# Optimization experiments

Hardware: AMD Instinct MI355X
Metric: run time of the kernel (lower is better)

Reference implementation:

```python
import jax, jax.numpy as jnp
import numpy as np
import math

DIM = 2048
N_HEADS = 16
HEAD_DIM = DIM // N_HEADS  # 128
SEQ = 2048
EPS = 1e-5
NEG = -1e9


def get_slopes(n):
    # n is a power of 2 here (16)
    start = 2.0 ** (-2.0 ** (-(math.log2(n) - 3)))
    return [start * start ** i for i in range(n)]


def setup_inputs() -> dict:
    key = jax.random.key(0)
    ks = jax.random.split(key, 6)
    x = jax.random.normal(ks[0], (1, SEQ, DIM), dtype=jnp.float32)
    # causal additive mask (large negative above diagonal)
    causal = jnp.tril(jnp.ones((SEQ, SEQ), dtype=bool))
    mask = jnp.where(causal, 0.0, NEG).astype(jnp.float32)[None, None]
    scale_w = 0.02
    wq = jax.random.normal(ks[1], (DIM, DIM), dtype=jnp.float32) * scale_w  # [in, out]
    wk = jax.random.normal(ks[2], (DIM, DIM), dtype=jnp.float32) * scale_w
    wv = jax.random.normal(ks[3], (DIM, DIM), dtype=jnp.float32) * scale_w
    wo = jax.random.normal(ks[4], (DIM, DIM), dtype=jnp.float32) * scale_w
    # AttentionPrior params: shape_init=1, scale_init='slope' (stored as log), loc_init=0
    shape = jnp.ones((1, N_HEADS, 1, 1), dtype=jnp.float32)
    scale = jnp.log(jnp.asarray(get_slopes(N_HEADS), dtype=jnp.float32)).reshape(1, N_HEADS, 1, 1)
    loc = jnp.zeros((1, N_HEADS, 1, 1), dtype=jnp.float32)
    return {"x": x, "mask": mask, "wq": wq, "wk": wk, "wv": wv, "wo": wo,
            "shape": shape, "scale": scale, "loc": loc, "start_pos": 0}


def _prior_bias(shape, scale, loc, seqlen, start_pos):
    q_pos = jnp.arange(seqlen, dtype=jnp.float32) + start_pos
    k_pos = jnp.arange(seqlen + start_pos, dtype=jnp.float32)
    dist = (k_pos[None, :] - q_pos[:, None])[None, None]  # [1,1,S,K]
    loc_t = jnp.exp(loc) - jnp.exp(-loc)
    z = (dist - loc_t) * jnp.exp(scale)  # [1,H,S,K]
    return -(jnp.abs(z) + EPS) ** shape


def reference(x, mask, wq, wk, wv, wo, shape, scale, loc, start_pos):
    bsz, seqlen, _ = x.shape
    q = (x @ wq).reshape(bsz, seqlen, N_HEADS, HEAD_DIM)
    k = (x @ wk).reshape(bsz, seqlen, N_HEADS, HEAD_DIM)
    v = (x @ wv).reshape(bsz, seqlen, N_HEADS, HEAD_DIM)
    # start_pos=0 prefill: cache slice == current keys/values
    scores = jnp.einsum('bqhd,bkhd->bhqk', q, k) / math.sqrt(HEAD_DIM)
    scores = scores + _prior_bias(shape, scale, loc, seqlen, start_pos)
    scores = scores + mask
    probs = jax.nn.softmax(scores.astype(jnp.float32), axis=-1).astype(q.dtype)
    out = jnp.einsum('bhqk,bkhd->bqhd', probs, v).reshape(bsz, seqlen, DIM)
    return out @ wo
```

## Files before the change

kernel.cpp:

```cpp
#include <hip/hip_runtime.h>
#include <hip/hip_bf16.h>
#include <stdint.h>


typedef unsigned short u16;
typedef unsigned int u32;

using bf16x8 = __attribute__((ext_vector_type(8))) __bf16;
using f32x4  = __attribute__((ext_vector_type(4))) float;

__device__ __forceinline__ u16 f2bf(float f) {
  union { float f; u32 u; } v; v.f = f;
  u32 r = (v.u + 0x7FFFu + ((v.u >> 16) & 1u)) >> 16;
  return (u16)r;
}

__device__ __forceinline__ float bf2f(u16 h) {
  union { u32 u; float f; } v; v.u = ((u32)h) << 16; return v.f;
}

__device__ __forceinline__ void gload16(const void* g, void* l) {
  __builtin_amdgcn_global_load_lds((const __attribute__((address_space(1))) void*)g,
                                   (__attribute__((address_space(3))) void*)l, 16, 0, 0);
}

__device__ __forceinline__ int cumchunks(int qt) {
  if (qt < 8)  return qt;
  if (qt < 16) return 8 + 2 * (qt - 8);
  if (qt < 24) return 24 + 3 * (qt - 16);
  return 48 + 4 * (qt - 24);
}

__global__ __launch_bounds__(256) void prep(const float* __restrict__ x, const float* __restrict__ wq,
                                            const float* __restrict__ wk, const float* __restrict__ wv,
                                            const float* __restrict__ wo,
                                            u16* __restrict__ xb, u16* __restrict__ wqkt,
                                            u16* __restrict__ wvt, u16* __restrict__ wot) {
  __shared__ float tile[32][33];
  const int z = blockIdx.z;
  const int t = threadIdx.x;
  if (z == 4) {
    int i = ((blockIdx.y * 64 + blockIdx.x) * 256 + t);
    float4 v = ((const float4*)x)[i];
    ushort4 o;
    o.x = f2bf(v.x); o.y = f2bf(v.y); o.z = f2bf(v.z); o.w = f2bf(v.w);
    ((ushort4*)xb)[i] = o;
    return;
  }
  const float* src = (z == 0) ? wq : (z == 1) ? wk : (z == 2) ? wv : wo;
  u16* dst = (z == 0) ? wqkt : (z == 1) ? (wqkt + 2048 * 2048) : (z == 2) ? wvt : wot;
  const int c0 = blockIdx.x * 32, r0 = blockIdx.y * 32;
  const int ci = t & 31, rj = t >> 5;
#pragma unroll
  for (int j = 0; j < 4; ++j)
    tile[rj + j * 8][ci] = src[(size_t)(r0 + rj + j * 8) * 2048 + c0 + ci];
  __syncthreads();
#pragma unroll
  for (int j = 0; j < 4; ++j) {
    int rr = rj + j * 8;
    dst[(size_t)(c0 + rr) * 2048 + r0 + ci] = f2bf(tile[ci][rr]);
  }
}

__global__ __launch_bounds__(256) void gemm_qkv(const u16* __restrict__ xb, const u16* __restrict__ wqkt,
                                                const u16* __restrict__ wvt,
                                                u16* __restrict__ qkc, u16* __restrict__ vtc) {
  __shared__ u16 lds[16384];
  int bid = blockIdx.x;
  const u16 *A, *Bt;
  u16* C;
  int N, bn, bm, scl_cols;
  if (bid < 512) { A = xb;  Bt = wqkt; C = qkc; N = 4096; bn = bid & 31; bm = bid >> 5; scl_cols = 2048; }
  else { bid -= 512; A = wvt; Bt = xb; C = vtc; N = 2048; bn = bid & 15; bm = bid >> 4; scl_cols = 0; }
  const int K = 2048;

  const int t = threadIdx.x;
  const int w = t >> 6, l = t & 63;
  const int wm = w >> 1, wn = w & 1;
  const int lrow = l & 15, lgrp = l >> 4;

  f32x4 acc[4][4] = {};

  for (int k0 = 0; k0 < K; k0 += 64) {
    if (k0) __syncthreads();
#pragma unroll
    for (int p = 0; p < 4; ++p) {
      int i = (p * 4 + w) * 64 + l;
      int r = i >> 3, u = i & 7;
      const u16* src = A + (size_t)(bm * 128 + r) * K + k0 + ((u ^ (r & 7)) << 3);
      gload16(src, (char*)lds + (p * 4 + w) * 1024);
    }
#pragma unroll
    for (int p = 0; p < 4; ++p) {
      int i = (p * 4 + w) * 64 + l;
      int r = i >> 3, u = i & 7;
      const u16* src = Bt + (size_t)(bn * 128 + r) * K + k0 + ((u ^ (r & 7)) << 3);
      gload16(src, (char*)lds + 16384 + (p * 4 + w) * 1024);
    }
    __syncthreads();

#pragma unroll
    for (int kc = 0; kc < 2; ++kc) {
      bf16x8 af[4], bfr[4];
#pragma unroll
      for (int mt = 0; mt < 4; ++mt) {
        int rho = wm * 64 + mt * 16 + lrow;
        int un = (kc * 4 + lgrp) ^ (rho & 7);
        af[mt] = *(const bf16x8*)((const char*)lds + rho * 128 + un * 16);
      }
#pragma unroll
      for (int nt = 0; nt < 4; ++nt) {
        int rho = wn * 64 + nt * 16 + lrow;
        int un = (kc * 4 + lgrp) ^ (rho & 7);
        bfr[nt] = *(const bf16x8*)((const char*)lds + 16384 + rho * 128 + un * 16);
      }
#pragma unroll
      for (int mt = 0; mt < 4; ++mt)
#pragma unroll
        for (int nt = 0; nt < 4; ++nt)
          acc[mt][nt] = __builtin_amdgcn_mfma_f32_16x16x32_bf16(af[mt], bfr[nt], acc[mt][nt], 0, 0, 0);
    }
  }

  const int row0 = bm * 128 + wm * 64;
  const int col0 = bn * 128 + wn * 64;
#pragma unroll
  for (int mt = 0; mt < 4; ++mt)
#pragma unroll
    for (int nt = 0; nt < 4; ++nt) {
      int col = col0 + nt * 16 + lrow;
      float s = (col < scl_cols) ? 0.08838834764831843f : 1.0f;
#pragma unroll
      for (int r = 0; r < 4; ++r) {
        int row = row0 + mt * 16 + lgrp * 4 + r;
        C[(size_t)row * N + col] = f2bf(acc[mt][nt][r] * s);
      }
    }
}

__global__ __launch_bounds__(256) void gemm_outk(const u16* __restrict__ A, const u16* __restrict__ Bt,
                                                 u16* __restrict__ P0, u16* __restrict__ P1) {
  __shared__ u16 lds[16384];
  const int b = blockIdx.x;
  const int z = b >> 8;
  const int bn = b & 15, bm = (b >> 4) & 15;
  u16* C = z ? P1 : P0;
  const int K = 2048;
  const int kbeg = z * 1024, kend = kbeg + 1024;

  const int t = threadIdx.x;
  const int w = t >> 6, l = t & 63;
  const int wm = w >> 1, wn = w & 1;
  const int lrow = l & 15, lgrp = l >> 4;

  f32x4 acc[4][4] = {};

  for (int k0 = kbeg; k0 < kend; k0 += 64) {
    if (k0 != kbeg) __syncthreads();
#pragma unroll
    for (int p = 0; p < 4; ++p) {
      int i = (p * 4 + w) * 64 + l;
      int r = i >> 3, u = i & 7;
      const u16* src = A + (size_t)(bm * 128 + r) * K + k0 + ((u ^ (r & 7)) << 3);
      gload16(src, (char*)lds + (p * 4 + w) * 1024);
    }
#pragma unroll
    for (int p = 0; p < 4; ++p) {
      int i = (p * 4 + w) * 64 + l;
      int r = i >> 3, u = i & 7;
      const u16* src = Bt + (size_t)(bn * 128 + r) * K + k0 + ((u ^ (r & 7)) << 3);
      gload16(src, (char*)lds + 16384 + (p * 4 + w) * 1024);
    }
    __syncthreads();

#pragma unroll
    for (int kc = 0; kc < 2; ++kc) {
      bf16x8 af[4], bfr[4];
#pragma unroll
      for (int mt = 0; mt < 4; ++mt) {
        int rho = wm * 64 + mt * 16 + lrow;
        int un = (kc * 4 + lgrp) ^ (rho & 7);
        af[mt] = *(const bf16x8*)((const char*)lds + rho * 128 + un * 16);
      }
#pragma unroll
      for (int nt = 0; nt < 4; ++nt) {
        int rho = wn * 64 + nt * 16 + lrow;
        int un = (kc * 4 + lgrp) ^ (rho & 7);
        bfr[nt] = *(const bf16x8*)((const char*)lds + 16384 + rho * 128 + un * 16);
      }
#pragma unroll
      for (int mt = 0; mt < 4; ++mt)
#pragma unroll
        for (int nt = 0; nt < 4; ++nt)
          acc[mt][nt] = __builtin_amdgcn_mfma_f32_16x16x32_bf16(af[mt], bfr[nt], acc[mt][nt], 0, 0, 0);
    }
  }

  const int row0 = bm * 128 + wm * 64;
  const int col0 = bn * 128 + wn * 64;
#pragma unroll
  for (int mt = 0; mt < 4; ++mt)
#pragma unroll
    for (int nt = 0; nt < 4; ++nt) {
      int col = col0 + nt * 16 + lrow;
#pragma unroll
      for (int r = 0; r < 4; ++r) {
        int row = row0 + mt * 16 + lgrp * 4 + r;
        C[(size_t)row * 2048 + col] = f2bf(acc[mt][nt][r]);
      }
    }
}

__global__ __launch_bounds__(256) void combine_out(const u16* __restrict__ P0, const u16* __restrict__ P1,
                                                   float* __restrict__ out) {
  const int i = blockIdx.x * 256 + threadIdx.x;
  uint4 a = ((const uint4*)P0)[i];
  uint4 b = ((const uint4*)P1)[i];
  float4 o0, o1;
  o0.x = bf2f(a.x & 0xFFFF) + bf2f(b.x & 0xFFFF); o0.y = bf2f(a.x >> 16) + bf2f(b.x >> 16);
  o0.z = bf2f(a.y & 0xFFFF) + bf2f(b.y & 0xFFFF); o0.w = bf2f(a.y >> 16) + bf2f(b.y >> 16);
  o1.x = bf2f(a.z & 0xFFFF) + bf2f(b.z & 0xFFFF); o1.y = bf2f(a.z >> 16) + bf2f(b.z >> 16);
  o1.z = bf2f(a.w & 0xFFFF) + bf2f(b.w & 0xFFFF); o1.w = bf2f(a.w >> 16) + bf2f(b.w >> 16);
  ((float4*)out)[i * 2]     = o0;
  ((float4*)out)[i * 2 + 1] = o1;
}

__global__ __launch_bounds__(256) void attn_part(const u16* __restrict__ QK, const u16* __restrict__ Vt,
                                                 u16* __restrict__ Opart, float* __restrict__ Lpart,
                                                 const float* __restrict__ g_shape,
                                                 const float* __restrict__ g_scale,
                                                 const float* __restrict__ g_loc,
                                                 const int* __restrict__ g_sp) {
  __shared__ u16 k_lds[2][4096];
  __shared__ u16 v_lds[2][4096];
  __shared__ u16 p_lds[4][640];

  const int raw = blockIdx.x;
  const int bid = (raw & 7) * 160 + (raw >> 3);
  const int h = bid / 80;
  const int rem = bid - h * 80;
  int qt, ch;
  if (rem < 8)       { qt = rem;                 ch = 0; }
  else if (rem < 24) { int r2 = rem - 8;  qt = 8  + (r2 >> 1); ch = r2 & 1; }
  else if (rem < 48) { int r3 = rem - 24; qt = 16 + r3 / 3;    ch = r3 - 3 * (r3 / 3); }
  else               { int r4 = rem - 48; qt = 24 + (r4 >> 2); ch = r4 & 3; }
  const int pid = bid;

  const int t = threadIdx.x, w = t >> 6, l = t & 63;
  const int lrow = l & 15, lgrp = l >> 4;

  const float sh = g_shape[h];
  const float es = __expf(g_scale[h]);
  const float lcv = g_loc[h];
  const float loc_t = __expf(lcv) - __expf(-lcv);
  const int sp = g_sp[0];
  const bool shape1 = (sh == 1.0f);

  const int qbase = qt * 64 + w * 16;

  bf16x8 qf[4];
  {
    const u16* qp = QK + (size_t)(qbase + lrow) * 4096 + h * 128 + lgrp * 8;
#pragma unroll
    for (int kc = 0; kc < 4; ++kc) qf[kc] = *(const bf16x8*)(qp + kc * 32);
  }

  f32x4 o[8] = {};
  float lr[4] = {0.0f, 0.0f, 0.0f, 0.0f};

  const int kstart = ch * 16;
  const int kend = min(kstart + 16, 2 * qt + 2);

#define STAGE_TILE(buf, kt_) do {                                                        \
    const int kv0s = (kt_) * 32;                                                         \
    _Pragma("unroll")                                                                    \
    for (int p = 0; p < 2; ++p) {                                                        \
      int i = p * 256 + t;                                                               \
      int r = i >> 4, u = i & 15;                                                        \
      const u16* src = QK + (size_t)(kv0s + r) * 4096 + 2048 + h * 128 + ((u ^ (r & 7)) << 3); \
      gload16(src, (char*)k_lds[buf] + (p * 256 + w * 64) * 16);                         \
    }                                                                                    \
    _Pragma("unroll")                                                                    \
    for (int p = 0; p < 2; ++p) {                                                        \
      int i = p * 256 + t;                                                               \
      int r = i >> 2, u = i & 3;                                                         \
      const u16* src = Vt + (size_t)(h * 128 + r) * 2048 + kv0s + ((u ^ ((r >> 2) & 3)) << 3); \
      gload16(src, (char*)v_lds[buf] + (p * 256 + w * 64) * 16);                         \
    }                                                                                    \
  } while (0)

  STAGE_TILE(0, kstart);
  __syncthreads();

  for (int kt = kstart; kt < kend; ++kt) {
    const int cur = (kt - kstart) & 1;
    if (kt + 1 < kend) STAGE_TILE(cur ^ 1, kt + 1);
    const int kv0 = kt * 32;

    f32x4 s4[2];
#pragma unroll
    for (int nc = 0; nc < 2; ++nc) s4[nc] = f32x4{-11.0f, -11.0f, -11.0f, -11.0f};
#pragma unroll
    for (int kc = 0; kc < 4; ++kc) {
#pragma unroll
      for (int nc = 0; nc < 2; ++nc) {
        int rho = nc * 16 + lrow;
        int un = (kc * 4 + lgrp) ^ (rho & 7);
        bf16x8 bk = *(const bf16x8*)((const char*)k_lds[cur] + rho * 256 + un * 16);
        s4[nc] = __builtin_amdgcn_mfma_f32_16x16x32_bf16(qf[kc], bk, s4[nc], 0, 0, 0);
      }
    }

    f32x4 p4[2];
    const bool need_mask = (kv0 + 31 > qbase + sp);
    if (shape1 && !need_mask) {
#pragma unroll
      for (int r = 0; r < 4; ++r) {
        const float fb = (float)(kv0 + lrow - (qbase + lgrp * 4 + r) - sp) - loc_t;
#pragma unroll
        for (int nc = 0; nc < 2; ++nc) {
          float u = fb + (float)(nc * 16);
          float p = __expf(fmaf(-es, fabsf(u), s4[nc][r]));
          p4[nc][r] = p;
          lr[r] += p;
        }
      }
    } else if (shape1) {
#pragma unroll
      for (int r = 0; r < 4; ++r) {
        const float fb = (float)(kv0 + lrow - (qbase + lgrp * 4 + r) - sp) - loc_t;
#pragma unroll
        for (int nc = 0; nc < 2; ++nc) {
          float u = fb + (float)(nc * 16);
          float p = __expf(fmaf(-es, fabsf(u), s4[nc][r]));
          p = (u + loc_t > 0.0f) ? 0.0f : p;
          p4[nc][r] = p;
          lr[r] += p;
        }
      }
    } else {
#pragma unroll
      for (int r = 0; r < 4; ++r) {
        const float fb = (float)(kv0 + lrow - (qbase + lgrp * 4 + r) - sp) - loc_t;
#pragma unroll
        for (int nc = 0; nc < 2; ++nc) {
          float u = fb + (float)(nc * 16);
          float az = fmaf(es, fabsf(u), 1e-5f);
          float p = __expf(s4[nc][r] - __powf(az, sh));
          p = (u + loc_t > 0.0f) ? 0.0f : p;
          p4[nc][r] = p;
          lr[r] += p;
        }
      }
    }

#pragma unroll
    for (int r = 0; r < 4; ++r)
#pragma unroll
      for (int nc = 0; nc < 2; ++nc)
        p_lds[w][(lgrp * 4 + r) * 40 + nc * 16 + lrow] = f2bf(p4[nc][r]);

    {
      bf16x8 pa = *(const bf16x8*)((const char*)p_lds[w] + lrow * 80 + lgrp * 16);
#pragma unroll
      for (int dc = 0; dc < 8; ++dc) {
        int rho = dc * 16 + lrow;
        int un = lgrp ^ ((rho >> 2) & 3);
        bf16x8 bv = *(const bf16x8*)((const char*)v_lds[cur] + rho * 64 + un * 16);
        o[dc] = __builtin_amdgcn_mfma_f32_16x16x32_bf16(pa, bv, o[dc], 0, 0, 0);
      }
    }

    __syncthreads();
  }
#undef STAGE_TILE

#pragma unroll
  for (int r = 0; r < 4; ++r)
#pragma unroll
    for (int msk = 1; msk <= 8; msk <<= 1) lr[r] += __shfl_xor(lr[r], msk);

  u16* ob = Opart + (size_t)pid * 8192;
#pragma unroll
  for (int dc = 0; dc < 8; ++dc) {
#pragma unroll
    for (int r = 0; r < 4; ++r) {
      int row = w * 16 + lgrp * 4 + r;
      ob[(size_t)row * 128 + dc * 16 + lrow] = f2bf(o[dc][r]);
    }
  }
  if (lrow == 0) {
#pragma unroll
    for (int r = 0; r < 4; ++r) {
      int row = w * 16 + lgrp * 4 + r;
      Lpart[(size_t)pid * 64 + row] = lr[r];
    }
  }
}

__global__ __launch_bounds__(256) void attn_merge(const u16* __restrict__ Opart,
                                                  const float* __restrict__ Lpart,
                                                  u16* __restrict__ AO) {
  const int bid = blockIdx.x;
  const int qt = bid & 31, h = bid >> 5;
  const int nch = (qt >> 3) + 1;
  const int base = h * 80 + cumchunks(qt);
  const int t = threadIdx.x;
  const int row = t >> 2;
  const int dseg = (t & 3) << 5;

  float acc[32] = {};
  float lstar = 0.0f;
#pragma unroll
  for (int i = 0; i < 4; ++i) {
    if (i < nch) {
      lstar += Lpart[(size_t)(base + i) * 64 + row];
      const ushort4* op = (const ushort4*)(Opart + (size_t)(base + i) * 8192 + row * 128 + dseg);
#pragma unroll
      for (int j = 0; j < 8; ++j) {
        ushort4 v = op[j];
        acc[j * 4 + 0] += bf2f(v.x); acc[j * 4 + 1] += bf2f(v.y);
        acc[j * 4 + 2] += bf2f(v.z); acc[j * 4 + 3] += bf2f(v.w);
      }
    }
  }
  const float inv = 1.0f / lstar;
  const int q_abs = qt * 64 + row;
  u16* dst = AO + (size_t)q_abs * 2048 + h * 128 + dseg;
#pragma unroll
  for (int j = 0; j < 8; ++j) {
    ushort4 ov;
    ov.x = f2bf(acc[j * 4 + 0] * inv); ov.y = f2bf(acc[j * 4 + 1] * inv);
    ov.z = f2bf(acc[j * 4 + 2] * inv); ov.w = f2bf(acc[j * 4 + 3] * inv);
    *(ushort4*)(dst + j * 4) = ov;
  }
}

extern "C" void kernel_launch(void* const* d_in, const int* in_sizes, int n_in,
                              void* d_out, int out_size, void* d_ws, size_t ws_size,
                              hipStream_t stream) {
  const float* x   = (const float*)d_in[0];
  const float* wq  = (const float*)d_in[2];
  const float* wk  = (const float*)d_in[3];
  const float* wv  = (const float*)d_in[4];
  const float* wo  = (const float*)d_in[5];
  const float* shp = (const float*)d_in[6];
  const float* scl = (const float*)d_in[7];
  const float* loc = (const float*)d_in[8];
  const int*   sp  = (const int*)d_in[9];

  char* ws = (char*)d_ws;
  u16*   xb    = (u16*)(ws);
  u16*   wqkt  = (u16*)(ws + (size_t)( 8u << 20));
  u16*   wvt   = (u16*)(ws + (size_t)(24u << 20));
  u16*   opart = (u16*)(ws);
  u16*   wot   = (u16*)(ws + (size_t)(40u << 20));
  u16*   qk    = (u16*)(ws + (size_t)(48u << 20));
  u16*   pc0   = (u16*)(ws + (size_t)(48u << 20));
  u16*   pc1   = (u16*)(ws + (size_t)(56u << 20));
  u16*   vt    = (u16*)(ws + (size_t)(64u << 20));
  u16*   ao    = (u16*)(ws + (size_t)(72u << 20));
  float* lpart = (float*)(ws + (size_t)(80u << 20));

  hipLaunchKernelGGL(prep, dim3(64, 64, 5), dim3(256), 0, stream,
                     x, wq, wk, wv, wo, xb, wqkt, wvt, wot);
  hipLaunchKernelGGL(gemm_qkv, dim3(768), dim3(256), 0, stream, xb, wqkt, wvt, qk, vt);
  hipLaunchKernelGGL(attn_part, dim3(1280), dim3(256), 0, stream,
                     qk, vt, opart, lpart, shp, scl, loc, sp);
  hipLaunchKernelGGL(attn_merge, dim3(512), dim3(256), 0, stream, opart, lpart, ao);
  hipLaunchKernelGGL(gemm_outk, dim3(512), dim3(256), 0, stream, ao, wot, pc0, pc1);
  hipLaunchKernelGGL(combine_out, dim3(2048), dim3(256), 0, stream, pc0, pc1, (float*)d_out);
}
```

Before: 166.3 us.

## Use 32x32 MFMA with 128-row query tiles in split attention

```diff
diff --git a/kernel.cpp b/kernel.cpp
--- a/kernel.cpp
+++ b/kernel.cpp
@@ -6,8 +6,9 @@
 typedef unsigned short u16;
 typedef unsigned int u32;
 
-using bf16x8 = __attribute__((ext_vector_type(8))) __bf16;
-using f32x4  = __attribute__((ext_vector_type(4))) float;
+using bf16x8  = __attribute__((ext_vector_type(8))) __bf16;
+using f32x4   = __attribute__((ext_vector_type(4))) float;
+using f32x16  = __attribute__((ext_vector_type(16))) float;
 
 __device__ __forceinline__ u16 f2bf(float f) {
   union { float f; u32 u; } v; v.f = f;
@@ -15,6 +16,10 @@
   return (u16)r;
 }
 
+__device__ __forceinline__ u16 f2bfn(float f) {
+  union { __bf16 b; u16 u; } c; c.b = (__bf16)f; return c.u;
+}
+
 __device__ __forceinline__ float bf2f(u16 h) {
   union { u32 u; float f; } v; v.u = ((u32)h) << 16; return v.f;
 }
@@ -24,11 +29,11 @@
                                    (__attribute__((address_space(3))) void*)l, 16, 0, 0);
 }
 
-__device__ __forceinline__ int cumchunks(int qt) {
-  if (qt < 8)  return qt;
-  if (qt < 16) return 8 + 2 * (qt - 8);
-  if (qt < 24) return 24 + 3 * (qt - 16);
-  return 48 + 4 * (qt - 24);
+__device__ __forceinline__ int cumch128(int qt) {
+  if (qt < 4)  return qt;
+  if (qt < 8)  return 4 + 2 * (qt - 4);
+  if (qt < 12) return 12 + 3 * (qt - 8);
+  return 24 + 4 * (qt - 12);
 }
 
 __global__ __launch_bounds__(256) void prep(const float* __restrict__ x, const float* __restrict__ wq,
@@ -233,21 +238,21 @@
                                                  const int* __restrict__ g_sp) {
   __shared__ u16 k_lds[2][4096];
   __shared__ u16 v_lds[2][4096];
-  __shared__ u16 p_lds[4][640];
+  __shared__ u16 p_lds[4][1280];
 
   const int raw = blockIdx.x;
-  const int bid = (raw & 7) * 160 + (raw >> 3);
-  const int h = bid / 80;
-  const int rem = bid - h * 80;
+  const int bid = (raw & 7) * 80 + (raw >> 3);
+  const int h = bid / 40;
+  const int rem = bid - h * 40;
   int qt, ch;
-  if (rem < 8)       { qt = rem;                 ch = 0; }
-  else if (rem < 24) { int r2 = rem - 8;  qt = 8  + (r2 >> 1); ch = r2 & 1; }
-  else if (rem < 48) { int r3 = rem - 24; qt = 16 + r3 / 3;    ch = r3 - 3 * (r3 / 3); }
-  else               { int r4 = rem - 48; qt = 24 + (r4 >> 2); ch = r4 & 3; }
+  if (rem < 4)       { qt = rem;                 ch = 0; }
+  else if (rem < 12) { int r2 = rem - 4;  qt = 4  + (r2 >> 1); ch = r2 & 1; }
+  else if (rem < 24) { int r3 = rem - 12; qt = 8  + r3 / 3;    ch = r3 - 3 * (r3 / 3); }
+  else               { int r4 = rem - 24; qt = 12 + (r4 >> 2); ch = r4 & 3; }
   const int pid = bid;
 
   const int t = threadIdx.x, w = t >> 6, l = t & 63;
-  const int lrow = l & 15, lgrp = l >> 4;
+  const int lc = l & 31, lh = l >> 5;
 
   const float sh = g_shape[h];
   const float es = __expf(g_scale[h]);
@@ -256,20 +261,22 @@
   const int sp = g_sp[0];
   const bool shape1 = (sh == 1.0f);
 
-  const int qbase = qt * 64 + w * 16;
-
-  bf16x8 qf[4];
+  const int qwave = qt * 128 + w * 32;
+
+  bf16x8 qf[8];
   {
-    const u16* qp = QK + (size_t)(qbase + lrow) * 4096 + h * 128 + lgrp * 8;
-#pragma unroll
-    for (int kc = 0; kc < 4; ++kc) qf[kc] = *(const bf16x8*)(qp + kc * 32);
-  }
-
-  f32x4 o[8] = {};
-  float lr[4] = {0.0f, 0.0f, 0.0f, 0.0f};
+    const u16* qp = QK + (size_t)(qwave + lc) * 4096 + h * 128 + lh * 8;
+#pragma unroll
+    for (int ks = 0; ks < 8; ++ks) qf[ks] = *(const bf16x8*)(qp + ks * 16);
+  }
+
+  f32x16 o[4] = {};
+  float lr[16];
+#pragma unroll
+  for (int r = 0; r < 16; ++r) lr[r] = 0.0f;
 
   const int kstart = ch * 16;
-  const int kend = min(kstart + 16, 2 * qt + 2);
+  const int kend = min(kstart + 16, 4 * qt + 4);
 
 #define STAGE_TILE(buf, kt_) do {                                                        \
     const int kv0s = (kt_) * 32;                                                         \
@@ -297,78 +304,62 @@
     if (kt + 1 < kend) STAGE_TILE(cur ^ 1, kt + 1);
     const int kv0 = kt * 32;
 
-    f32x4 s4[2];
-#pragma unroll
-    for (int nc = 0; nc < 2; ++nc) s4[nc] = f32x4{-11.0f, -11.0f, -11.0f, -11.0f};
-#pragma unroll
-    for (int kc = 0; kc < 4; ++kc) {
-#pragma unroll
-      for (int nc = 0; nc < 2; ++nc) {
-        int rho = nc * 16 + lrow;
-        int un = (kc * 4 + lgrp) ^ (rho & 7);
-        bf16x8 bk = *(const bf16x8*)((const char*)k_lds[cur] + rho * 256 + un * 16);
-        s4[nc] = __builtin_amdgcn_mfma_f32_16x16x32_bf16(qf[kc], bk, s4[nc], 0, 0, 0);
-      }
-    }
-
-    f32x4 p4[2];
-    const bool need_mask = (kv0 + 31 > qbase + sp);
+    f32x16 s;
+#pragma unroll
+    for (int r = 0; r < 16; ++r) s[r] = -11.0f;
+#pragma unroll
+    for (int ks = 0; ks < 8; ++ks) {
+      int un = (ks * 2 + lh) ^ (lc & 7);
+      bf16x8 bk = *(const bf16x8*)((const char*)k_lds[cur] + lc * 256 + un * 16);
+      s = __builtin_amdgcn_mfma_f32_32x32x16_bf16(qf[ks], bk, s, 0, 0, 0);
+    }
+
+    const float fdb = (float)(kv0 + lc - (qwave + 4 * lh) - sp);
+    const float fb = fdb - loc_t;
+    const bool need_mask = (kv0 + 31 > qwave + sp);
     if (shape1 && !need_mask) {
 #pragma unroll
-      for (int r = 0; r < 4; ++r) {
-        const float fb = (float)(kv0 + lrow - (qbase + lgrp * 4 + r) - sp) - loc_t;
-#pragma unroll
-        for (int nc = 0; nc < 2; ++nc) {
-          float u = fb + (float)(nc * 16);
-          float p = __expf(fmaf(-es, fabsf(u), s4[nc][r]));
-          p4[nc][r] = p;
-          lr[r] += p;
-        }
+      for (int r = 0; r < 16; ++r) {
+        const float rowoff = (float)((r & 3) + 8 * (r >> 2));
+        float u = fb - rowoff;
+        float p = __expf(fmaf(-es, fabsf(u), s[r]));
+        lr[r] += p;
+        p_lds[w][((r & 3) + 8 * (r >> 2) + 4 * lh) * 40 + lc] = f2bfn(p);
       }
     } else if (shape1) {
 #pragma unroll
-      for (int r = 0; r < 4; ++r) {
-        const float fb = (float)(kv0 + lrow - (qbase + lgrp * 4 + r) - sp) - loc_t;
-#pragma unroll
-        for (int nc = 0; nc < 2; ++nc) {
-          float u = fb + (float)(nc * 16);
-          float p = __expf(fmaf(-es, fabsf(u), s4[nc][r]));
-          p = (u + loc_t > 0.0f) ? 0.0f : p;
-          p4[nc][r] = p;
-          lr[r] += p;
-        }
+      for (int r = 0; r < 16; ++r) {
+        const float rowoff = (float)((r & 3) + 8 * (r >> 2));
+        float u = fb - rowoff;
+        float p = __expf(fmaf(-es, fabsf(u), s[r]));
+        p = (fdb > rowoff) ? 0.0f : p;
+        lr[r] += p;
+        p_lds[w][((r & 3) + 8 * (r >> 2) + 4 * lh) * 40 + lc] = f2bfn(p);
       }
     } else {
 #pragma unroll
-      for (int r = 0; r < 4; ++r) {
-        const float fb = (float)(kv0 + lrow - (qbase + lgrp * 4 + r) - sp) - loc_t;
-#pragma unroll
-        for (int nc = 0; nc < 2; ++nc) {
-          float u = fb + (float)(nc * 16);
-          float az = fmaf(es, fabsf(u), 1e-5f);
-          float p = __expf(s4[nc][r] - __powf(az, sh));
-          p = (u + loc_t > 0.0f) ? 0.0f : p;
-          p4[nc][r] = p;
-          lr[r] += p;
-        }
-      }
-    }
-
-#pragma unroll
-    for (int r = 0; r < 4; ++r)
-#pragma unroll
-      for (int nc = 0; nc < 2; ++nc)
-        p_lds[w][(lgrp * 4 + r) * 40 + nc * 16 + lrow] = f2bf(p4[nc][r]);
-
-    {
-      bf16x8 pa = *(const bf16x8*)((const char*)p_lds[w] + lrow * 80 + lgrp * 16);
-#pragma unroll
-      for (int dc = 0; dc < 8; ++dc) {
-        int rho = dc * 16 + lrow;
-        int un = lgrp ^ ((rho >> 2) & 3);
-        bf16x8 bv = *(const bf16x8*)((const char*)v_lds[cur] + rho * 64 + un * 16);
-        o[dc] = __builtin_amdgcn_mfma_f32_16x16x32_bf16(pa, bv, o[dc], 0, 0, 0);
-      }
+      for (int r = 0; r < 16; ++r) {
+        const float rowoff = (float)((r & 3) + 8 * (r >> 2));
+        float u = fb - rowoff;
+        float az = fmaf(es, fabsf(u), 1e-5f);
+        float p = __expf(s[r] - __powf(az, sh));
+        p = (fdb > rowoff) ? 0.0f : p;
+        lr[r] += p;
+        p_lds[w][((r & 3) + 8 * (r >> 2) + 4 * lh) * 40 + lc] = f2bfn(p);
+      }
+    }
+
+    bf16x8 pa0 = *(const bf16x8*)((const char*)p_lds[w] + lc * 80 + lh * 16);
+    bf16x8 pa1 = *(const bf16x8*)((const char*)p_lds[w] + lc * 80 + 32 + lh * 16);
+#pragma unroll
+    for (int dc = 0; dc < 4; ++dc) {
+      int row0 = dc * 32 + lc;
+      int un0 = (lh) ^ ((row0 >> 2) & 3);
+      int un1 = (2 + lh) ^ ((row0 >> 2) & 3);
+      bf16x8 bv0 = *(const bf16x8*)((const char*)v_lds[cur] + row0 * 64 + un0 * 16);
+      bf16x8 bv1 = *(const bf16x8*)((const char*)v_lds[cur] + row0 * 64 + un1 * 16);
+      o[dc] = __builtin_amdgcn_mfma_f32_32x32x16_bf16(pa0, bv0, o[dc], 0, 0, 0);
+      o[dc] = __builtin_amdgcn_mfma_f32_32x32x16_bf16(pa1, bv1, o[dc], 0, 0, 0);
     }
 
     __syncthreads();
@@ -376,24 +367,25 @@
 #undef STAGE_TILE
 
 #pragma unroll
-  for (int r = 0; r < 4; ++r)
-#pragma unroll
-    for (int msk = 1; msk <= 8; msk <<= 1) lr[r] += __shfl_xor(lr[r], msk);
-
-  u16* ob = Opart + (size_t)pid * 8192;
-#pragma unroll
-  for (int dc = 0; dc < 8; ++dc) {
-#pragma unroll
-    for (int r = 0; r < 4; ++r) {
-      int row = w * 16 + lgrp * 4 + r;
-      ob[(size_t)row * 128 + dc * 16 + lrow] = f2bf(o[dc][r]);
-    }
-  }
-  if (lrow == 0) {
-#pragma unroll
-    for (int r = 0; r < 4; ++r) {
-      int row = w * 16 + lgrp * 4 + r;
-      Lpart[(size_t)pid * 64 + row] = lr[r];
+  for (int r = 0; r < 16; ++r) {
+#pragma unroll
+    for (int msk = 1; msk <= 16; msk <<= 1) lr[r] += __shfl_xor(lr[r], msk);
+  }
+
+  u16* ob = Opart + (size_t)pid * 16384;
+#pragma unroll
+  for (int dc = 0; dc < 4; ++dc) {
+#pragma unroll
+    for (int r = 0; r < 16; ++r) {
+      int row = w * 32 + (r & 3) + 8 * (r >> 2) + 4 * lh;
+      ob[(size_t)row * 128 + dc * 32 + lc] = f2bfn(o[dc][r]);
+    }
+  }
+  if (lc == 0) {
+#pragma unroll
+    for (int r = 0; r < 16; ++r) {
+      int row = w * 32 + (r & 3) + 8 * (r >> 2) + 4 * lh;
+      Lpart[(size_t)pid * 128 + row] = lr[r];
     }
   }
 }
@@ -402,22 +394,22 @@
                                                   const float* __restrict__ Lpart,
                                                   u16* __restrict__ AO) {
   const int bid = blockIdx.x;
-  const int qt = bid & 31, h = bid >> 5;
-  const int nch = (qt >> 3) + 1;
-  const int base = h * 80 + cumchunks(qt);
+  const int qt = bid & 15, h = bid >> 4;
+  const int nch = (qt >> 2) + 1;
+  const int base = h * 40 + cumch128(qt);
   const int t = threadIdx.x;
-  const int row = t >> 2;
-  const int dseg = (t & 3) << 5;
-
-  float acc[32] = {};
+  const int row = t >> 1;
+  const int dseg = (t & 1) << 6;
+
+  float acc[64] = {};
   float lstar = 0.0f;
 #pragma unroll
   for (int i = 0; i < 4; ++i) {
     if (i < nch) {
-      lstar += Lpart[(size_t)(base + i) * 64 + row];
-      const ushort4* op = (const ushort4*)(Opart + (size_t)(base + i) * 8192 + row * 128 + dseg);
-#pragma unroll
-      for (int j = 0; j < 8; ++j) {
+      lstar += Lpart[(size_t)(base + i) * 128 + row];
+      const ushort4* op = (const ushort4*)(Opart + (size_t)(base + i) * 16384 + row * 128 + dseg);
+#pragma unroll
+      for (int j = 0; j < 16; ++j) {
         ushort4 v = op[j];
         acc[j * 4 + 0] += bf2f(v.x); acc[j * 4 + 1] += bf2f(v.y);
         acc[j * 4 + 2] += bf2f(v.z); acc[j * 4 + 3] += bf2f(v.w);
@@ -425,10 +417,10 @@
     }
   }
   const float inv = 1.0f / lstar;
-  const int q_abs = qt * 64 + row;
+  const int q_abs = qt * 128 + row;
   u16* dst = AO + (size_t)q_abs * 2048 + h * 128 + dseg;
 #pragma unroll
-  for (int j = 0; j < 8; ++j) {
+  for (int j = 0; j < 16; ++j) {
     ushort4 ov;
     ov.x = f2bf(acc[j * 4 + 0] * inv); ov.y = f2bf(acc[j * 4 + 1] * inv);
     ov.z = f2bf(acc[j * 4 + 2] * inv); ov.w = f2bf(acc[j * 4 + 3] * inv);
@@ -465,9 +457,9 @@
   hipLaunchKernelGGL(prep, dim3(64, 64, 5), dim3(256), 0, stream,
                      x, wq, wk, wv, wo, xb, wqkt, wvt, wot);
   hipLaunchKernelGGL(gemm_qkv, dim3(768), dim3(256), 0, stream, xb, wqkt, wvt, qk, vt);
-  hipLaunchKernelGGL(attn_part, dim3(1280), dim3(256), 0, stream,
+  hipLaunchKernelGGL(attn_part, dim3(640), dim3(256), 0, stream,
                      qk, vt, opart, lpart, shp, scl, loc, sp);
-  hipLaunchKernelGGL(attn_merge, dim3(512), dim3(256), 0, stream, opart, lpart, ao);
+  hipLaunchKernelGGL(attn_merge, dim3(256), dim3(256), 0, stream, opart, lpart, ao);
   hipLaunchKernelGGL(gemm_outk, dim3(512), dim3(256), 0, stream, ao, wot, pc0, pc1);
   hipLaunchKernelGGL(combine_out, dim3(2048), dim3(256), 0, stream, pc0, pc1, (float*)d_out);
 }
```

New measurement: 171.0 us. +2.8%, slower.

## Replace split-KV attention plus merge with one full-row kernel in longest-first order

Applied to the files above, without the earlier changes.

```diff
diff --git a/kernel.cpp b/kernel.cpp
--- a/kernel.cpp
+++ b/kernel.cpp
@@ -15,6 +15,10 @@
   return (u16)r;
 }
 
+__device__ __forceinline__ u16 f2bfn(float f) {
+  union { __bf16 b; u16 u; } c; c.b = (__bf16)f; return c.u;
+}
+
 __device__ __forceinline__ float bf2f(u16 h) {
   union { u32 u; float f; } v; v.u = ((u32)h) << 16; return v.f;
 }
@@ -22,13 +26,6 @@
 __device__ __forceinline__ void gload16(const void* g, void* l) {
   __builtin_amdgcn_global_load_lds((const __attribute__((address_space(1))) void*)g,
                                    (__attribute__((address_space(3))) void*)l, 16, 0, 0);
-}
-
-__device__ __forceinline__ int cumchunks(int qt) {
-  if (qt < 8)  return qt;
-  if (qt < 16) return 8 + 2 * (qt - 8);
-  if (qt < 24) return 24 + 3 * (qt - 16);
-  return 48 + 4 * (qt - 24);
 }
 
 __global__ __launch_bounds__(256) void prep(const float* __restrict__ x, const float* __restrict__ wq,
@@ -225,26 +222,19 @@
   ((float4*)out)[i * 2 + 1] = o1;
 }
 
-__global__ __launch_bounds__(256) void attn_part(const u16* __restrict__ QK, const u16* __restrict__ Vt,
-                                                 u16* __restrict__ Opart, float* __restrict__ Lpart,
-                                                 const float* __restrict__ g_shape,
-                                                 const float* __restrict__ g_scale,
-                                                 const float* __restrict__ g_loc,
-                                                 const int* __restrict__ g_sp) {
+__global__ __launch_bounds__(256) void attn_fullrow(const u16* __restrict__ QK, const u16* __restrict__ Vt,
+                                                    u16* __restrict__ AO,
+                                                    const float* __restrict__ g_shape,
+                                                    const float* __restrict__ g_scale,
+                                                    const float* __restrict__ g_loc,
+                                                    const int* __restrict__ g_sp) {
   __shared__ u16 k_lds[2][4096];
   __shared__ u16 v_lds[2][4096];
   __shared__ u16 p_lds[4][640];
 
-  const int raw = blockIdx.x;
-  const int bid = (raw & 7) * 160 + (raw >> 3);
-  const int h = bid / 80;
-  const int rem = bid - h * 80;
-  int qt, ch;
-  if (rem < 8)       { qt = rem;                 ch = 0; }
-  else if (rem < 24) { int r2 = rem - 8;  qt = 8  + (r2 >> 1); ch = r2 & 1; }
-  else if (rem < 48) { int r3 = rem - 24; qt = 16 + r3 / 3;    ch = r3 - 3 * (r3 / 3); }
-  else               { int r4 = rem - 48; qt = 24 + (r4 >> 2); ch = r4 & 3; }
-  const int pid = bid;
+  const int bid = blockIdx.x;
+  const int qt = 31 - (bid >> 4);
+  const int h = bid & 15;
 
   const int t = threadIdx.x, w = t >> 6, l = t & 63;
   const int lrow = l & 15, lgrp = l >> 4;
@@ -268,8 +258,7 @@
   f32x4 o[8] = {};
   float lr[4] = {0.0f, 0.0f, 0.0f, 0.0f};
 
-  const int kstart = ch * 16;
-  const int kend = min(kstart + 16, 2 * qt + 2);
+  const int kend = 2 * qt + 2;
 
 #define STAGE_TILE(buf, kt_) do {                                                        \
     const int kv0s = (kt_) * 32;                                                         \
@@ -289,11 +278,11 @@
     }                                                                                    \
   } while (0)
 
-  STAGE_TILE(0, kstart);
+  STAGE_TILE(0, 0);
   __syncthreads();
 
-  for (int kt = kstart; kt < kend; ++kt) {
-    const int cur = (kt - kstart) & 1;
+  for (int kt = 0; kt < kend; ++kt) {
+    const int cur = kt & 1;
     if (kt + 1 < kend) STAGE_TILE(cur ^ 1, kt + 1);
     const int kv0 = kt * 32;
 
@@ -358,7 +347,7 @@
     for (int r = 0; r < 4; ++r)
 #pragma unroll
       for (int nc = 0; nc < 2; ++nc)
-        p_lds[w][(lgrp * 4 + r) * 40 + nc * 16 + lrow] = f2bf(p4[nc][r]);
+        p_lds[w][(lgrp * 4 + r) * 40 + nc * 16 + lrow] = f2bfn(p4[nc][r]);
 
     {
       bf16x8 pa = *(const bf16x8*)((const char*)p_lds[w] + lrow * 80 + lgrp * 16);
@@ -375,64 +364,21 @@
   }
 #undef STAGE_TILE
 
-#pragma unroll
-  for (int r = 0; r < 4; ++r)
+  float inv[4];
+#pragma unroll
+  for (int r = 0; r < 4; ++r) {
 #pragma unroll
     for (int msk = 1; msk <= 8; msk <<= 1) lr[r] += __shfl_xor(lr[r], msk);
-
-  u16* ob = Opart + (size_t)pid * 8192;
+    inv[r] = 1.0f / lr[r];
+  }
+
 #pragma unroll
   for (int dc = 0; dc < 8; ++dc) {
 #pragma unroll
     for (int r = 0; r < 4; ++r) {
-      int row = w * 16 + lgrp * 4 + r;
-      ob[(size_t)row * 128 + dc * 16 + lrow] = f2bf(o[dc][r]);
-    }
-  }
-  if (lrow == 0) {
-#pragma unroll
-    for (int r = 0; r < 4; ++r) {
-      int row = w * 16 + lgrp * 4 + r;
-      Lpart[(size_t)pid * 64 + row] = lr[r];
-    }
-  }
-}
-
-__global__ __launch_bounds__(256) void attn_merge(const u16* __restrict__ Opart,
-                                                  const float* __restrict__ Lpart,
-                                                  u16* __restrict__ AO) {
-  const int bid = blockIdx.x;
-  const int qt = bid & 31, h = bid >> 5;
-  const int nch = (qt >> 3) + 1;
-  const int base = h * 80 + cumchunks(qt);
-  const int t = threadIdx.x;
-  const int row = t >> 2;
-  const int dseg = (t & 3) << 5;
-
-  float acc[32] = {};
-  float lstar = 0.0f;
-#pragma unroll
-  for (int i = 0; i < 4; ++i) {
-    if (i < nch) {
-      lstar += Lpart[(size_t)(base + i) * 64 + row];
-      const ushort4* op = (const ushort4*)(Opart + (size_t)(base + i) * 8192 + row * 128 + dseg);
-#pragma unroll
-      for (int j = 0; j < 8; ++j) {
-        ushort4 v = op[j];
-        acc[j * 4 + 0] += bf2f(v.x); acc[j * 4 + 1] += bf2f(v.y);
-        acc[j * 4 + 2] += bf2f(v.z); acc[j * 4 + 3] += bf2f(v.w);
-      }
-    }
-  }
-  const float inv = 1.0f / lstar;
-  const int q_abs = qt * 64 + row;
-  u16* dst = AO + (size_t)q_abs * 2048 + h * 128 + dseg;
-#pragma unroll
-  for (int j = 0; j < 8; ++j) {
-    ushort4 ov;
-    ov.x = f2bf(acc[j * 4 + 0] * inv); ov.y = f2bf(acc[j * 4 + 1] * inv);
-    ov.z = f2bf(acc[j * 4 + 2] * inv); ov.w = f2bf(acc[j * 4 + 3] * inv);
-    *(ushort4*)(dst + j * 4) = ov;
+      int row = qbase + lgrp * 4 + r;
+      AO[(size_t)row * 2048 + h * 128 + dc * 16 + lrow] = f2bfn(o[dc][r] * inv[r]);
+    }
   }
 }
 
@@ -453,21 +399,18 @@
   u16*   xb    = (u16*)(ws);
   u16*   wqkt  = (u16*)(ws + (size_t)( 8u << 20));
   u16*   wvt   = (u16*)(ws + (size_t)(24u << 20));
-  u16*   opart = (u16*)(ws);
   u16*   wot   = (u16*)(ws + (size_t)(40u << 20));
   u16*   qk    = (u16*)(ws + (size_t)(48u << 20));
   u16*   pc0   = (u16*)(ws + (size_t)(48u << 20));
   u16*   pc1   = (u16*)(ws + (size_t)(56u << 20));
   u16*   vt    = (u16*)(ws + (size_t)(64u << 20));
   u16*   ao    = (u16*)(ws + (size_t)(72u << 20));
-  float* lpart = (float*)(ws + (size_t)(80u << 20));
 
   hipLaunchKernelGGL(prep, dim3(64, 64, 5), dim3(256), 0, stream,
                      x, wq, wk, wv, wo, xb, wqkt, wvt, wot);
   hipLaunchKernelGGL(gemm_qkv, dim3(768), dim3(256), 0, stream, xb, wqkt, wvt, qk, vt);
-  hipLaunchKernelGGL(attn_part, dim3(1280), dim3(256), 0, stream,
-                     qk, vt, opart, lpart, shp, scl, loc, sp);
-  hipLaunchKernelGGL(attn_merge, dim3(512), dim3(256), 0, stream, opart, lpart, ao);
+  hipLaunchKernelGGL(attn_fullrow, dim3(512), dim3(256), 0, stream,
+                     qk, vt, ao, shp, scl, loc, sp);
   hipLaunchKernelGGL(gemm_outk, dim3(512), dim3(256), 0, stream, ao, wot, pc0, pc1);
   hipLaunchKernelGGL(combine_out, dim3(2048), dim3(256), 0, stream, pc0, pc1, (float*)d_out);
 }
```

Measured after the change: 180.4 us. 1.08x slower.
